# Optimization experiments

Measured on AMD Instinct MI355X. Metric: run time of the kernel, lower is better.

## Reference

```python
import jax, jax.numpy as jnp
import numpy as np

EPS = 1e-06  # min_gamma_value

def spectral_function(eigvals):
    # reciprocal spectral function: f(lambda) = 1 / lambda (lambda >= EPS by construction)
    return 1.0 / eigvals

def setup_inputs() -> dict:
    key = jax.random.key(0)
    x = jax.random.normal(key, (4, 64, 16, 128, 128), dtype=jnp.float32)  # [B, C, K, H, W]
    return {"x": x}

def reference(x):
    # [B, C, K, H, W] -> [B, H, W, K, C]
    m = jnp.transpose(x, (0, 3, 4, 2, 1))
    K = m.shape[-2]
    # per-pixel KxK Gram matrix, regularized
    sym = jnp.einsum('bhwkc,bhwlc->bhwkl', m, m) + EPS * jnp.eye(K, dtype=m.dtype)
    eigvals, eigvecs = jnp.linalg.eigh(sym)          # eigvals [B,H,W,K], eigvecs [B,H,W,K,K]
    f = spectral_function(eigvals)                    # elementwise spectral map
    # V diag(f) V^T
    out = jnp.einsum('bhwik,bhwk,bhwjk->bhwij', eigvecs, f, eigvecs)
    return out
```

## Files before the change

kernel.cpp:

```cpp
#include <hip/hip_runtime.h>
#include <utility>


#define EPSR 1e-6f

__device__ __host__ constexpr int rowof(int t) {
    int i = 0;
    while ((i + 1) * (i + 2) / 2 <= t) ++i;
    return i;
}
__device__ __host__ constexpr int colof(int t) { return t - rowof(t) * (rowof(t) + 1) / 2; }

__device__ __forceinline__ constexpr int tidx(int i, int j) {
    return i * (i + 1) / 2 + j;
}

#define GLOAD_LDS16(gp, lp)                                                       \
    __builtin_amdgcn_global_load_lds(                                             \
        (const __attribute__((address_space(1))) void*)(gp),                      \
        (__attribute__((address_space(3))) void*)(lp), 16, 0, 0)


template<int P>
__device__ __forceinline__ void fma_pair(const float (&m)[16], float& a) {
    a = fmaf(m[rowof(P)], m[colof(P)], a);
}

template<int G, int... TT>
__device__ __forceinline__ void fma_group(const float (&m)[16], float (&acc)[68],
                                          std::integer_sequence<int, TT...>) {
    (fma_pair<G * 68 + TT>(m, acc[TT]), ...);
}

template<int G>
__device__ __forceinline__ void chunk_fma4(const float* __restrict__ buf, int lane,
                                           float (&acc)[68]) {
    #pragma unroll
    for (int cs = 0; cs < 4; ++cs) {
        float m[16];
        #pragma unroll
        for (int k = 0; k < 16; ++k) m[k] = buf[(cs * 16 + k) * 64 + lane];
        fma_group<G>(m, acc, std::make_integer_sequence<int, 68>{});
    }
}

template<int P>
__device__ __forceinline__ void store_tri_pair(float* __restrict__ tri, int lane, float v) {
    constexpr bool diag = (rowof(P) == colof(P));
    tri[P * 67 + lane] = diag ? (v + EPSR) : v;
}

template<int G, int... TT>
__device__ __forceinline__ void store_tri_group(float* __restrict__ tri, int lane,
                                                const float (&acc)[68],
                                                std::integer_sequence<int, TT...>) {
    (store_tri_pair<G * 68 + TT>(tri, lane, acc[TT]), ...);
}


union SMem {
    float stage[2][4096];
    float tri[136 * 67];
};

__global__ __launch_bounds__(128, 2)
void fused_gram_inv(const float* __restrict__ x, float* __restrict__ out) {
    __shared__ __align__(16) SMem sm;

    const int tid = threadIdx.x;
    const int lane = tid & 63;
    const int wv = tid >> 6;
    const int p0 = blockIdx.x * 64;
    const int b = blockIdx.x >> 8;
    const int hw0 = p0 & 16383;

    const float* gbase = x + (size_t)b * 16777216 + hw0
                           + (size_t)(lane >> 4) * 16384 + (size_t)(lane & 15) * 4;

    float acc[68];
    #pragma unroll
    for (int t = 0; t < 68; ++t) acc[t] = 0.0f;

    auto STAGE = [&](int bufi, int c0) {
        #pragma unroll
        for (int s = 0; s < 2; ++s) {
            const int cs = wv + 2 * s;
            #pragma unroll
            for (int q = 0; q < 4; ++q) {
                GLOAD_LDS16(gbase + (size_t)(c0 + cs) * 262144 + (size_t)(q * 4) * 16384,
                            &sm.stage[bufi][(cs * 16 + q * 4) * 64]);
            }
        }
    };

    STAGE(0, 0);
    for (int t = 0; t < 16; ++t) {
        __syncthreads();
        if (t < 15) STAGE((t + 1) & 1, 4 * (t + 1));
        const float* buf = sm.stage[t & 1];
        if (wv == 0) chunk_fma4<0>(buf, lane, acc);
        else         chunk_fma4<1>(buf, lane, acc);
    }
    __syncthreads();

    if (wv == 0) store_tri_group<0>(sm.tri, lane, acc, std::make_integer_sequence<int, 68>{});
    else         store_tri_group<1>(sm.tri, lane, acc, std::make_integer_sequence<int, 68>{});
    __syncthreads();

    if (wv == 0) {
        float s[136];
        #pragma unroll
        for (int t = 0; t < 136; ++t) s[t] = sm.tri[t * 67 + lane];

        #pragma unroll
        for (int j = 0; j < 16; ++j) {
            float d = s[tidx(j, j)];
            #pragma unroll
            for (int q = 0; q < j; ++q) d = fmaf(-s[tidx(j, q)], s[tidx(j, q)], d);
            const float invd = 1.0f / sqrtf(d);
            s[tidx(j, j)] = invd;
            #pragma unroll
            for (int i = j + 1; i < 16; ++i) {
                float v = s[tidx(i, j)];
                #pragma unroll
                for (int q = 0; q < j; ++q) v = fmaf(-s[tidx(i, q)], s[tidx(j, q)], v);
                s[tidx(i, j)] = v * invd;
            }
        }

        #pragma unroll
        for (int j = 0; j < 16; ++j) {
            #pragma unroll
            for (int i = j + 1; i < 16; ++i) {
                float sum = s[tidx(i, j)] * s[tidx(j, j)];
                #pragma unroll
                for (int q = j + 1; q < i; ++q)
                    sum = fmaf(s[tidx(i, q)], s[tidx(q, j)], sum);
                s[tidx(i, j)] = -s[tidx(i, i)] * sum;
            }
        }

        #pragma unroll
        for (int j = 0; j < 16; ++j) {
            #pragma unroll
            for (int i = j; i < 16; ++i) {
                float sum = 0.0f;
                #pragma unroll
                for (int q = i; q < 16; ++q)
                    sum = fmaf(s[tidx(q, i)], s[tidx(q, j)], sum);
                s[tidx(i, j)] = sum;
            }
        }

        #pragma unroll
        for (int t = 0; t < 136; ++t) sm.tri[t * 67 + lane] = s[t];
    }
    __syncthreads();

    const int e0 = tid;
    const int e1 = tid + 128;
    const int i0 = e0 >> 4, j0 = e0 & 15;
    const int h0 = i0 > j0 ? i0 : j0, l0 = i0 + j0 - h0;
    const int trow0 = h0 * (h0 + 1) / 2 + l0;
    const int i1 = e1 >> 4, j1 = e1 & 15;
    const int h1 = i1 > j1 ? i1 : j1, l1 = i1 + j1 - h1;
    const int trow1 = h1 * (h1 + 1) / 2 + l1;

    float* gout = out + (size_t)p0 * 256;
    #pragma unroll 8
    for (int a = 0; a < 64; ++a) {
        gout[(size_t)a * 256 + e0] = sm.tri[trow0 * 67 + a];
        gout[(size_t)a * 256 + e1] = sm.tri[trow1 * 67 + a];
    }
}

extern "C" void kernel_launch(void* const* d_in, const int* in_sizes, int n_in,
                              void* d_out, int out_size, void* d_ws, size_t ws_size,
                              hipStream_t stream) {
    const float* x = (const float*)d_in[0];
    float* out = (float*)d_out;
    hipLaunchKernelGGL(fused_gram_inv, dim3(1024), dim3(128), 0, stream, x, out);
}
```

Baseline: 78.34 us.

## Load Gram inputs directly from global memory instead of LDS double-buffering

Drops the double-buffered global_load_lds staging pipeline and the per-chunk block barriers. Each wave now reads its 16 K-values per channel straight from global memory into registers and accumulates its share of the Gram matrix. Both waves read the same data, so global load traffic doubles, though the second read may hit cache. Without explicit prefetching, the change relies on the compiler and hardware to hide load latency, and register pressure may rise.

```diff
diff --git a/kernel.cpp b/kernel.cpp
--- a/kernel.cpp
+++ b/kernel.cpp
@@ -15,11 +15,6 @@
     return i * (i + 1) / 2 + j;
 }
 
-#define GLOAD_LDS16(gp, lp)                                                       \
-    __builtin_amdgcn_global_load_lds(                                             \
-        (const __attribute__((address_space(1))) void*)(gp),                      \
-        (__attribute__((address_space(3))) void*)(lp), 16, 0, 0)
-
 
 template<int P>
 __device__ __forceinline__ void fma_pair(const float (&m)[16], float& a) {
@@ -33,13 +28,14 @@
 }
 
 template<int G>
-__device__ __forceinline__ void chunk_fma4(const float* __restrict__ buf, int lane,
-                                           float (&acc)[68]) {
-    #pragma unroll
-    for (int cs = 0; cs < 4; ++cs) {
+__device__ __forceinline__ void gram_direct(const float* __restrict__ xb,
+                                            float (&acc)[68]) {
+    #pragma unroll 2
+    for (int c = 0; c < 64; ++c) {
         float m[16];
         #pragma unroll
-        for (int k = 0; k < 16; ++k) m[k] = buf[(cs * 16 + k) * 64 + lane];
+        for (int k = 0; k < 16; ++k)
+            m[k] = xb[(size_t)c * 262144 + (size_t)k * 16384];
         fma_group<G>(m, acc, std::make_integer_sequence<int, 68>{});
     }
 }
@@ -58,14 +54,9 @@
 }
 
 
-union SMem {
-    float stage[2][4096];
-    float tri[136 * 67];
-};
-
 __global__ __launch_bounds__(128, 2)
 void fused_gram_inv(const float* __restrict__ x, float* __restrict__ out) {
-    __shared__ __align__(16) SMem sm;
+    __shared__ float tri[136 * 67];
 
     const int tid = threadIdx.x;
     const int lane = tid & 63;
@@ -74,43 +65,23 @@
     const int b = blockIdx.x >> 8;
     const int hw0 = p0 & 16383;
 
-    const float* gbase = x + (size_t)b * 16777216 + hw0
-                           + (size_t)(lane >> 4) * 16384 + (size_t)(lane & 15) * 4;
+    const float* xb = x + (size_t)b * 16777216 + hw0 + lane;
 
     float acc[68];
     #pragma unroll
     for (int t = 0; t < 68; ++t) acc[t] = 0.0f;
 
-    auto STAGE = [&](int bufi, int c0) {
-        #pragma unroll
-        for (int s = 0; s < 2; ++s) {
-            const int cs = wv + 2 * s;
-            #pragma unroll
-            for (int q = 0; q < 4; ++q) {
-                GLOAD_LDS16(gbase + (size_t)(c0 + cs) * 262144 + (size_t)(q * 4) * 16384,
-                            &sm.stage[bufi][(cs * 16 + q * 4) * 64]);
-            }
-        }
-    };
+    if (wv == 0) gram_direct<0>(xb, acc);
+    else         gram_direct<1>(xb, acc);
 
-    STAGE(0, 0);
-    for (int t = 0; t < 16; ++t) {
-        __syncthreads();
-        if (t < 15) STAGE((t + 1) & 1, 4 * (t + 1));
-        const float* buf = sm.stage[t & 1];
-        if (wv == 0) chunk_fma4<0>(buf, lane, acc);
-        else         chunk_fma4<1>(buf, lane, acc);
-    }
-    __syncthreads();
-
-    if (wv == 0) store_tri_group<0>(sm.tri, lane, acc, std::make_integer_sequence<int, 68>{});
-    else         store_tri_group<1>(sm.tri, lane, acc, std::make_integer_sequence<int, 68>{});
+    if (wv == 0) store_tri_group<0>(tri, lane, acc, std::make_integer_sequence<int, 68>{});
+    else         store_tri_group<1>(tri, lane, acc, std::make_integer_sequence<int, 68>{});
     __syncthreads();
 
     if (wv == 0) {
         float s[136];
         #pragma unroll
-        for (int t = 0; t < 136; ++t) s[t] = sm.tri[t * 67 + lane];
+        for (int t = 0; t < 136; ++t) s[t] = tri[t * 67 + lane];
 
         #pragma unroll
         for (int j = 0; j < 16; ++j) {
@@ -153,7 +124,7 @@
         }
 
         #pragma unroll
-        for (int t = 0; t < 136; ++t) sm.tri[t * 67 + lane] = s[t];
+        for (int t = 0; t < 136; ++t) tri[t * 67 + lane] = s[t];
     }
     __syncthreads();
 
@@ -169,8 +140,8 @@
     float* gout = out + (size_t)p0 * 256;
     #pragma unroll 8
     for (int a = 0; a < 64; ++a) {
-        gout[(size_t)a * 256 + e0] = sm.tri[trow0 * 67 + a];
-        gout[(size_t)a * 256 + e1] = sm.tri[trow1 * 67 + a];
+        gout[(size_t)a * 256 + e0] = tri[trow0 * 67 + a];
+        gout[(size_t)a * 256 + e1] = tri[trow1 * 67 + a];
     }
 }
 
```

Result: slower. 82.75 us (+5.6%).

## Deepen load pipeline to four smaller stage buffers with manual vmcnt waits

Applied to the files above, without the earlier changes.

Replaces the double-buffered 4-channel staging with a 4-deep ring of 2-channel stages that keeps three async global-to-LDS loads in flight. Partial s_waitcnt vmcnt counts plus a raw s_barrier replace the full __syncthreads, so the next loads can issue before earlier ones have drained. The aim is to hide global memory latency better in this bandwidth-bound Gram accumulation. In exchange there are twice as many barriers, and correctness now depends on the hand-tuned vmcnt values matching the number of outstanding loads per wave.

```diff
diff --git a/kernel.cpp b/kernel.cpp
--- a/kernel.cpp
+++ b/kernel.cpp
@@ -33,13 +33,13 @@
 }
 
 template<int G>
-__device__ __forceinline__ void chunk_fma4(const float* __restrict__ buf, int lane,
+__device__ __forceinline__ void chunk_fma2(const float* __restrict__ buf, int lane,
                                            float (&acc)[68]) {
     #pragma unroll
-    for (int cs = 0; cs < 4; ++cs) {
+    for (int cs = 0; cs < 2; ++cs) {
         float m[16];
         #pragma unroll
-        for (int k = 0; k < 16; ++k) m[k] = buf[(cs * 16 + k) * 64 + lane];
+        for (int k = 0; k < 16; ++k) m[k] = buf[cs * 1024 + k * 64 + lane];
         fma_group<G>(m, acc, std::make_integer_sequence<int, 68>{});
     }
 }
@@ -59,7 +59,7 @@
 
 
 union SMem {
-    float stage[2][4096];
+    float stage[4][2048];
     float tri[136 * 67];
 };
 
@@ -81,25 +81,39 @@
     #pragma unroll
     for (int t = 0; t < 68; ++t) acc[t] = 0.0f;
 
-    auto STAGE = [&](int bufi, int c0) {
+    auto STAGE = [&](int bufi, int t) {
+        const float* gp = gbase + (size_t)(2 * t + wv) * 262144;
         #pragma unroll
-        for (int s = 0; s < 2; ++s) {
-            const int cs = wv + 2 * s;
-            #pragma unroll
-            for (int q = 0; q < 4; ++q) {
-                GLOAD_LDS16(gbase + (size_t)(c0 + cs) * 262144 + (size_t)(q * 4) * 16384,
-                            &sm.stage[bufi][(cs * 16 + q * 4) * 64]);
-            }
+        for (int q = 0; q < 4; ++q) {
+            GLOAD_LDS16(gp + (size_t)(q * 4) * 16384,
+                        &sm.stage[bufi][(wv * 16 + q * 4) * 64]);
         }
     };
 
     STAGE(0, 0);
-    for (int t = 0; t < 16; ++t) {
-        __syncthreads();
-        if (t < 15) STAGE((t + 1) & 1, 4 * (t + 1));
-        const float* buf = sm.stage[t & 1];
-        if (wv == 0) chunk_fma4<0>(buf, lane, acc);
-        else         chunk_fma4<1>(buf, lane, acc);
+    STAGE(1, 1);
+    STAGE(2, 2);
+    for (int t = 0; t < 30; ++t) {
+        asm volatile("s_waitcnt vmcnt(8)" ::: "memory");
+        __builtin_amdgcn_s_barrier();
+        if (t < 29) STAGE((t + 3) & 3, t + 3);
+        const float* buf = sm.stage[t & 3];
+        if (wv == 0) chunk_fma2<0>(buf, lane, acc);
+        else         chunk_fma2<1>(buf, lane, acc);
+    }
+    {
+        asm volatile("s_waitcnt vmcnt(4)" ::: "memory");
+        __builtin_amdgcn_s_barrier();
+        const float* buf = sm.stage[30 & 3];
+        if (wv == 0) chunk_fma2<0>(buf, lane, acc);
+        else         chunk_fma2<1>(buf, lane, acc);
+    }
+    {
+        asm volatile("s_waitcnt vmcnt(0)" ::: "memory");
+        __builtin_amdgcn_s_barrier();
+        const float* buf = sm.stage[31 & 3];
+        if (wv == 0) chunk_fma2<0>(buf, lane, acc);
+        else         chunk_fma2<1>(buf, lane, acc);
     }
     __syncthreads();
 
```

Result: no change. 78.29 us (-0.1%).

## Process 128 pixels per block with 256 threads and half-size channel chunks

Applied to the files above, without the earlier changes.

Doubles the pixels per block from 64 to 128 and uses four waves, two pixel halves times two Gram-entry groups, while halving the channel chunk per stage to keep the stage buffer the same size. The grid shrinks from 1024 to 512 blocks. The goal is more waves per CU and wider contiguous global loads (32 lanes x 16 bytes per row instead of 16 x 16). In exchange it runs twice as many sync iterations, and the triangle buffer grows to 136x131 floats, about 71 KB of LDS, which may cut resident blocks per CU. Only half the waves still do the inversion.

```diff
diff --git a/kernel.cpp b/kernel.cpp
--- a/kernel.cpp
+++ b/kernel.cpp
@@ -3,6 +3,7 @@
 
 
 #define EPSR 1e-6f
+#define TS2 131
 
 __device__ __host__ constexpr int rowof(int t) {
     int i = 0;
@@ -33,84 +34,85 @@
 }
 
 template<int G>
-__device__ __forceinline__ void chunk_fma4(const float* __restrict__ buf, int lane,
+__device__ __forceinline__ void chunk_fma2(const float* __restrict__ buf, int px,
                                            float (&acc)[68]) {
     #pragma unroll
-    for (int cs = 0; cs < 4; ++cs) {
+    for (int cs = 0; cs < 2; ++cs) {
         float m[16];
         #pragma unroll
-        for (int k = 0; k < 16; ++k) m[k] = buf[(cs * 16 + k) * 64 + lane];
+        for (int k = 0; k < 16; ++k) m[k] = buf[cs * 2048 + k * 128 + px];
         fma_group<G>(m, acc, std::make_integer_sequence<int, 68>{});
     }
 }
 
 template<int P>
-__device__ __forceinline__ void store_tri_pair(float* __restrict__ tri, int lane, float v) {
+__device__ __forceinline__ void store_tri_pair(float* __restrict__ tri, int px, float v) {
     constexpr bool diag = (rowof(P) == colof(P));
-    tri[P * 67 + lane] = diag ? (v + EPSR) : v;
+    tri[P * TS2 + px] = diag ? (v + EPSR) : v;
 }
 
 template<int G, int... TT>
-__device__ __forceinline__ void store_tri_group(float* __restrict__ tri, int lane,
+__device__ __forceinline__ void store_tri_group(float* __restrict__ tri, int px,
                                                 const float (&acc)[68],
                                                 std::integer_sequence<int, TT...>) {
-    (store_tri_pair<G * 68 + TT>(tri, lane, acc[TT]), ...);
+    (store_tri_pair<G * 68 + TT>(tri, px, acc[TT]), ...);
 }
 
 
 union SMem {
     float stage[2][4096];
-    float tri[136 * 67];
+    float tri[136 * TS2];
 };
 
-__global__ __launch_bounds__(128, 2)
+__global__ __launch_bounds__(256, 2)
 void fused_gram_inv(const float* __restrict__ x, float* __restrict__ out) {
     __shared__ __align__(16) SMem sm;
 
     const int tid = threadIdx.x;
     const int lane = tid & 63;
     const int wv = tid >> 6;
-    const int p0 = blockIdx.x * 64;
-    const int b = blockIdx.x >> 8;
+    const int G = wv & 1;
+    const int ph = wv >> 1;
+    const int px = ph * 64 + lane;
+    const int p0 = blockIdx.x * 128;
+    const int b = blockIdx.x >> 7;
     const int hw0 = p0 & 16383;
 
     const float* gbase = x + (size_t)b * 16777216 + hw0
-                           + (size_t)(lane >> 4) * 16384 + (size_t)(lane & 15) * 4;
+                           + (size_t)(lane >> 5) * 16384 + (size_t)(lane & 31) * 4;
 
     float acc[68];
     #pragma unroll
     for (int t = 0; t < 68; ++t) acc[t] = 0.0f;
 
     auto STAGE = [&](int bufi, int c0) {
+        const float* gp = gbase + (size_t)(c0 + ph) * 262144
+                                + (size_t)(G * 8) * 16384;
         #pragma unroll
-        for (int s = 0; s < 2; ++s) {
-            const int cs = wv + 2 * s;
-            #pragma unroll
-            for (int q = 0; q < 4; ++q) {
-                GLOAD_LDS16(gbase + (size_t)(c0 + cs) * 262144 + (size_t)(q * 4) * 16384,
-                            &sm.stage[bufi][(cs * 16 + q * 4) * 64]);
-            }
+        for (int q = 0; q < 4; ++q) {
+            GLOAD_LDS16(gp + (size_t)(q * 2) * 16384,
+                        &sm.stage[bufi][ph * 2048 + (G * 8 + q * 2) * 128]);
         }
     };
 
     STAGE(0, 0);
-    for (int t = 0; t < 16; ++t) {
+    for (int t = 0; t < 32; ++t) {
         __syncthreads();
-        if (t < 15) STAGE((t + 1) & 1, 4 * (t + 1));
+        if (t < 31) STAGE((t + 1) & 1, 2 * (t + 1));
         const float* buf = sm.stage[t & 1];
-        if (wv == 0) chunk_fma4<0>(buf, lane, acc);
-        else         chunk_fma4<1>(buf, lane, acc);
+        if (G == 0) chunk_fma2<0>(buf, px, acc);
+        else        chunk_fma2<1>(buf, px, acc);
     }
     __syncthreads();
 
-    if (wv == 0) store_tri_group<0>(sm.tri, lane, acc, std::make_integer_sequence<int, 68>{});
-    else         store_tri_group<1>(sm.tri, lane, acc, std::make_integer_sequence<int, 68>{});
+    if (G == 0) store_tri_group<0>(sm.tri, px, acc, std::make_integer_sequence<int, 68>{});
+    else        store_tri_group<1>(sm.tri, px, acc, std::make_integer_sequence<int, 68>{});
     __syncthreads();
 
-    if (wv == 0) {
+    if (G == 0) {
         float s[136];
         #pragma unroll
-        for (int t = 0; t < 136; ++t) s[t] = sm.tri[t * 67 + lane];
+        for (int t = 0; t < 136; ++t) s[t] = sm.tri[t * TS2 + px];
 
         #pragma unroll
         for (int j = 0; j < 16; ++j) {
@@ -153,24 +155,19 @@
         }
 
         #pragma unroll
-        for (int t = 0; t < 136; ++t) sm.tri[t * 67 + lane] = s[t];
+        for (int t = 0; t < 136; ++t) sm.tri[t * TS2 + px] = s[t];
     }
     __syncthreads();
 
-    const int e0 = tid;
-    const int e1 = tid + 128;
-    const int i0 = e0 >> 4, j0 = e0 & 15;
-    const int h0 = i0 > j0 ? i0 : j0, l0 = i0 + j0 - h0;
-    const int trow0 = h0 * (h0 + 1) / 2 + l0;
-    const int i1 = e1 >> 4, j1 = e1 & 15;
-    const int h1 = i1 > j1 ? i1 : j1, l1 = i1 + j1 - h1;
-    const int trow1 = h1 * (h1 + 1) / 2 + l1;
-
+    const int e = tid;
+    const int i = e >> 4, j = e & 15;
+    const int hi = i > j ? i : j;
+    const int lo = i + j - hi;
+    const int trow = hi * (hi + 1) / 2 + lo;
     float* gout = out + (size_t)p0 * 256;
     #pragma unroll 8
-    for (int a = 0; a < 64; ++a) {
-        gout[(size_t)a * 256 + e0] = sm.tri[trow0 * 67 + a];
-        gout[(size_t)a * 256 + e1] = sm.tri[trow1 * 67 + a];
+    for (int a = 0; a < 128; ++a) {
+        gout[(size_t)a * 256 + e] = sm.tri[trow * TS2 + a];
     }
 }
 
@@ -179,5 +176,5 @@
                               hipStream_t stream) {
     const float* x = (const float*)d_in[0];
     float* out = (float*)d_out;
-    hipLaunchKernelGGL(fused_gram_inv, dim3(1024), dim3(128), 0, stream, x, out);
+    hipLaunchKernelGGL(fused_gram_inv, dim3(512), dim3(256), 0, stream, x, out);
 }
```

New measurement: 70.89 us. -9.5%, faster.
